# Kernel optimization log

Measured on AMD Instinct MI355X. Metric: run time of the kernel, lower is better.

## Reference

```python
import jax, jax.numpy as jnp
import numpy as np

N = 50000      # nodes
E = 800000     # edges
D_IN = 128     # irreps_in dim
SH = 16        # irreps_sh dim (lmax=3)
EA = 16        # edge_attr_dim
H = 8          # num_heads
DQ = 64        # irreps_query dim (8 per head)
DK = 64        # irreps_key dim (8 per head)
DV = 128       # irreps_out dim (16 per head)
HID = 64       # radial MLP hidden


def setup_inputs() -> dict:
    key = jax.random.key(0)
    ks = jax.random.split(key, 20)
    g = lambda k, shape, fan: jax.random.normal(k, shape, jnp.float32) / np.sqrt(fan)
    return {
        "node_attr": jax.random.normal(ks[0], (N, D_IN), jnp.float32),
        "edge_attr": jax.random.normal(ks[1], (E, EA), jnp.float32),
        "edge_sh": jax.random.normal(ks[2], (E, SH), jnp.float32),
        # h_q linear
        "Wq": g(ks[3], (D_IN, DQ), D_IN),
        # h_k conv: depthwise SH mixing, channel-mixing linear, radial MLP gate
        "Wang_k": g(ks[4], (D_IN, SH), SH),
        "Wlin_k": g(ks[5], (D_IN, DK), D_IN),
        "W1k": g(ks[6], (EA, HID), EA),
        "b1k": jnp.zeros((HID,), jnp.float32),
        "W2k": g(ks[7], (HID, DK), HID),
        # h_v conv
        "Wang_v": g(ks[8], (D_IN, SH), SH),
        "Wlin_v": g(ks[9], (D_IN, DV), D_IN),
        "W1v": g(ks[10], (EA, HID), EA),
        "b1v": jnp.zeros((HID,), jnp.float32),
        "W2v": g(ks[11], (HID, DV), HID),
        # FullyConnectedTensorProduct(query_per_head, key_per_head, '0e') -> weighted bilinear dot
        "Wdot": g(ks[12], (DQ // H, DK // H), DQ // H),
        # lin_out
        "Wout": g(ks[13], (DV, DV), DV),
        "edge_index": jax.random.randint(ks[14], (2, E), 0, N, jnp.int64),
    }


def _conv_per_edge(x_src, edge_attr, edge_sh, Wang, Wlin, W1, b1, W2):
    # depthwise tensor product of node feats with edge SH, channel mix, radial gate
    rad = jax.nn.relu(edge_attr @ W1 + b1) @ W2          # [E, Dout]
    g = edge_sh @ Wang.T                                  # [E, D_IN]
    return ((x_src * g) @ Wlin) * rad                     # [E, Dout]


def reference(node_attr, edge_attr, edge_sh, Wq, Wang_k, Wlin_k, W1k, b1k, W2k,
              Wang_v, Wlin_v, W1v, b1v, W2v, Wdot, Wout, edge_index):
    src, dst = edge_index[0], edge_index[1]
    n = node_attr.shape[0]
    e = src.shape[0]

    q = (node_attr @ Wq).reshape(n, H, DQ // H)           # [N,H,dq]
    x_src = node_attr[src]                                # gather [E,D_IN]
    k = _conv_per_edge(x_src, edge_attr, edge_sh, Wang_k, Wlin_k, W1k, b1k, W2k).reshape(e, H, DK // H)
    v = _conv_per_edge(x_src, edge_attr, edge_sh, Wang_v, Wlin_v, W1v, b1v, W2v).reshape(e, H, DV // H)

    # TP 'dot' to scalars: weighted bilinear per head
    alpha = jnp.einsum('ehq,qk,ehk->eh', q[dst], Wdot, k)  # [E,H]

    # scatter_softmax over incoming edges of each dst node
    amax = jax.ops.segment_max(alpha, dst, num_segments=n)  # [N,H]
    ealpha = jnp.exp(alpha - amax[dst])
    denom = jax.ops.segment_sum(ealpha, dst, num_segments=n)
    attn = ealpha / denom[dst]                              # [E,H]

    # weighted scatter-sum of values
    out = jax.ops.segment_sum(attn[..., None] * v, dst, num_segments=n)  # [N,H,dv]
    return out.reshape(n, DV) @ Wout
```

## Files before the change

### kernel.cpp

```cpp
#include <hip/hip_runtime.h>
#include <stdint.h>

#define NN 50000
#define NE 800000
#define STRIP 49

typedef unsigned int u32;
typedef uint16_t u16;

__device__ __forceinline__ float b2f(u16 u){ return __builtin_bit_cast(float, (u32)((u32)u << 16)); }
__device__ __forceinline__ float b2f_lo(u32 p){ return __builtin_bit_cast(float, p << 16); }
__device__ __forceinline__ float b2f_hi(u32 p){ return __builtin_bit_cast(float, p & 0xffff0000u); }
__device__ __forceinline__ u32 f2b_bits(float f){ u32 u = __builtin_bit_cast(u32, f); return (u + 0x7fffu + ((u >> 16) & 1u)) >> 16; }
__device__ __forceinline__ u16 f2b(float f){ return (u16)f2b_bits(f); }
__device__ __forceinline__ u32 packb(float lo, float hi){ return f2b_bits(lo) | (f2b_bits(hi) << 16); }

typedef __bf16 bf16x2 __attribute__((ext_vector_type(2)));
#if defined(__has_builtin)
#if __has_builtin(__builtin_amdgcn_fdot2_f32_bf16)
#define HAVE_DOT2_BUILTIN 1
#endif
#endif

#ifdef HAVE_DOT2_BUILTIN
__device__ __forceinline__ float dot2b(u32 a, u32 b, float c){
  return __builtin_amdgcn_fdot2_f32_bf16(__builtin_bit_cast(bf16x2, a),
                                         __builtin_bit_cast(bf16x2, b), c, false);
}
#else
__device__ __forceinline__ float dot2b(u32 a, u32 b, float c){
  c = fmaf(b2f_lo(a), b2f_lo(b), c);
  return fmaf(b2f_hi(a), b2f_hi(b), c);
}
#endif

typedef __attribute__((ext_vector_type(8))) short short8;
typedef __attribute__((ext_vector_type(4))) float f32x4;
__device__ __forceinline__ f32x4 mf32(uint4 a, uint4 b, f32x4 c){
  return __builtin_amdgcn_mfma_f32_16x16x32_bf16(
      __builtin_bit_cast(short8, a), __builtin_bit_cast(short8, b), c, 0, 0, 0);
}

#define OFF_WANG_V 0
#define OFF_W1_V   5120
#define OFF_WLIN_V 7680
#define OFF_W2_V   25088
#define OFF_WANG_K 34304
#define OFF_W1_K   39424
#define OFF_WLIN_K 41984
#define OFF_W2_K   50688
#define OFF_WOUT   55296
#define OFF_WQD    72704
#define WT_TOTAL   81408

__global__ __launch_bounds__(256) void zero_kernel(int* __restrict__ counts,
                                                   int* __restrict__ edge_ids)
{
  int i = blockIdx.x * 256 + threadIdx.x;
  if (i < NN) counts[i] = 0;
  if (i < NE) edge_ids[i] = 0;
}

__global__ __launch_bounds__(256) void prep_w_kernel(
    const float* __restrict__ Wang_v, const float* __restrict__ W1_v,
    const float* __restrict__ Wlin_v, const float* __restrict__ W2_v,
    const float* __restrict__ Wang_k, const float* __restrict__ W1_k,
    const float* __restrict__ Wlin_k, const float* __restrict__ W2_k,
    const float* __restrict__ Wout, const float* __restrict__ Wq,
    const float* __restrict__ Wdot,
    u16* __restrict__ wt)
{
  int idx = blockIdx.x * 256 + threadIdx.x;
  if (idx >= WT_TOTAL) return;
  float val = 0.f;
  if (idx < OFF_W1_V) {
    int l = idx - OFF_WANG_V, n = l / 40, k = l % 40;
    if (k < 16) val = Wang_v[n * 16 + k];
  } else if (idx < OFF_WLIN_V) {
    int l = idx - OFF_W1_V, n = l / 40, k = l % 40;
    if (k < 16) val = W1_v[k * 64 + n];
  } else if (idx < OFF_W2_V) {
    int l = idx - OFF_WLIN_V, n = l / 136, k = l % 136;
    if (k < 128) val = Wlin_v[k * 128 + n];
  } else if (idx < OFF_WANG_K) {
    int l = idx - OFF_W2_V, n = l / 72, k = l % 72;
    if (k < 64) val = W2_v[k * 128 + n];
  } else if (idx < OFF_W1_K) {
    int l = idx - OFF_WANG_K, n = l / 40, k = l % 40;
    if (k < 16) val = Wang_k[n * 16 + k];
  } else if (idx < OFF_WLIN_K) {
    int l = idx - OFF_W1_K, n = l / 40, k = l % 40;
    if (k < 16) val = W1_k[k * 64 + n];
  } else if (idx < OFF_W2_K) {
    int l = idx - OFF_WLIN_K, n = l / 136, k = l % 136;
    if (k < 128) val = Wlin_k[k * 64 + n];
  } else if (idx < OFF_WOUT) {
    int l = idx - OFF_W2_K, n = l / 72, k = l % 72;
    if (k < 64) val = W2_k[k * 64 + n];
  } else if (idx < OFF_WQD) {
    int l = idx - OFF_WOUT, n = l / 136, k = l % 136;
    if (k < 128) val = Wout[k * 128 + n];
  } else {
    int l = idx - OFF_WQD, n = l / 136, k = l % 136;
    if (k < 128) {
      int h = n >> 3, r = n & 7;
      float s = 0.f;
#pragma unroll
      for (int i = 0; i < 8; ++i) s += Wq[k * 64 + h * 8 + i] * Wdot[i * 8 + r];
      val = s;
    }
  }
  wt[idx] = f2b(val);
}

__global__ __launch_bounds__(256) void qw_kernel(const float* __restrict__ node_attr,
                                                 const u16* __restrict__ wt,
                                                 u16* __restrict__ qw)
{
  __shared__ __align__(16) u16 sX[64 * 136];
  uint4* sX4 = (uint4*)sX;
  u32* sX32 = (u32*)sX;
  const uint4* wt4 = (const uint4*)wt;
  const int tid = threadIdx.x, wv = tid >> 6, lane = tid & 63, lq = lane >> 4, ln = lane & 15;
  const int n0 = blockIdx.x * 64;
  uint4 rB[4];
#pragma unroll
  for (int ks = 0; ks < 4; ++ks) rB[ks] = wt4[9088 + (wv * 16 + ln) * 17 + ks * 4 + lq];
  {
    int row = tid >> 2, q4 = tid & 3;
    int n = n0 + row;
    bool valid = n < NN;
    const float4* xp = (const float4*)(node_attr + (size_t)(valid ? n : 0) * 128);
#pragma unroll
    for (int i = 0; i < 8; ++i) {
      float4 v = valid ? xp[q4 * 8 + i] : make_float4(0.f, 0.f, 0.f, 0.f);
      sX32[row * 68 + (q4 * 8 + i) * 2]     = packb(v.x, v.y);
      sX32[row * 68 + (q4 * 8 + i) * 2 + 1] = packb(v.z, v.w);
    }
  }
  __syncthreads();
  const f32x4 z4 = {0.f, 0.f, 0.f, 0.f};
  int col = wv * 16 + ln;
#pragma unroll
  for (int et = 0; et < 4; ++et) {
    f32x4 acc = z4;
#pragma unroll
    for (int ks = 0; ks < 4; ++ks) acc = mf32(sX4[(et * 16 + ln) * 17 + ks * 4 + lq], rB[ks], acc);
#pragma unroll
    for (int r = 0; r < 4; ++r) {
      int rr = n0 + et * 16 + lq * 4 + r;
      if (rr < NN) qw[(size_t)rr * 64 + col] = f2b(acc[r]);
    }
  }
}

__global__ __launch_bounds__(256, 2) void conv_fused_kernel(
    const float* __restrict__ node_attr, const float* __restrict__ edge_attr,
    const float* __restrict__ edge_sh, const int* __restrict__ edge_index,
    const float* __restrict__ b1v, const float* __restrict__ b1k,
    const u16* __restrict__ wt, const u16* __restrict__ qw,
    u16* __restrict__ v_out, float* __restrict__ alpha)
{
  __shared__ __align__(16) u16 sE[5120];
  __shared__ __align__(16) u16 sTv[64 * 136];
  __shared__ __align__(16) u16 sTk[64 * 136];
  __shared__ __align__(16) u16 sHv[64 * 72];
  __shared__ __align__(16) u16 sHk[64 * 72];
  uint4* sE4 = (uint4*)sE;   u32* sE32 = (u32*)sE;
  uint4* sTv4 = (uint4*)sTv; uint4* sTk4 = (uint4*)sTk;
  uint4* sHv4 = (uint4*)sHv; uint4* sHk4 = (uint4*)sHk;
  const uint4* wt4 = (const uint4*)wt;

  const int tid = threadIdx.x;
  const int wv = tid >> 6, lane = tid & 63, lq = lane >> 4, ln = lane & 15;
  const int e0 = blockIdx.x * 64;
  const int nA = wv * 16 + ln, nB = (wv + 4) * 16 + ln;

  int el = tid >> 2, p = tid & 3;
  int dq = edge_index[NE + e0 + el]; if ((u32)dq >= NN) dq = 0;
  const uint4* qptr = (const uint4*)(qw + (size_t)dq * 64 + p * 16);
  uint4 q0 = qptr[0], q1 = qptr[1];

  uint4 rWangV0 = wt4[nA * 5 + lq],        rWangV1 = wt4[nB * 5 + lq];
  uint4 rW1V    = wt4[640 + nA * 5 + lq];
  uint4 rWangK0 = wt4[4288 + nA * 5 + lq], rWangK1 = wt4[4288 + nB * 5 + lq];
  uint4 rW1K    = wt4[4928 + nA * 5 + lq];
  uint4 rWlinV[2][4], rWlinK[4], rW2V[2][2], rW2K[2];
#pragma unroll
  for (int ks = 0; ks < 4; ++ks) {
    rWlinV[0][ks] = wt4[960 + nA * 17 + ks * 4 + lq];
    rWlinV[1][ks] = wt4[960 + nB * 17 + ks * 4 + lq];
    rWlinK[ks]    = wt4[5248 + nA * 17 + ks * 4 + lq];
  }
#pragma unroll
  for (int ks = 0; ks < 2; ++ks) {
    rW2V[0][ks] = wt4[3136 + nA * 9 + ks * 4 + lq];
    rW2V[1][ks] = wt4[3136 + nB * 9 + ks * 4 + lq];
    rW2K[ks]    = wt4[6336 + nA * 9 + ks * 4 + lq];
  }
  float biasV = b1v[nA], biasK = b1k[nA];

  int srcs[4][4];
#pragma unroll
  for (int et = 0; et < 4; ++et)
#pragma unroll
    for (int r = 0; r < 4; ++r) {
      int s = edge_index[e0 + et * 16 + lq * 4 + r];
      if ((u32)s >= NN) s = 0;
      srcs[et][r] = s;
    }
  float xf[2][4][4];
#pragma unroll
  for (int c = 0; c < 2; ++c) {
    int col = (wv + 4 * c) * 16 + ln;
#pragma unroll
    for (int et = 0; et < 4; ++et)
#pragma unroll
      for (int r = 0; r < 4; ++r)
        xf[c][et][r] = node_attr[(size_t)srcs[et][r] * 128 + col];
  }

  {
    int r = tid >> 2, kq = tid & 3;
    float4 ea = ((const float4*)(edge_attr + (size_t)(e0 + r) * 16))[kq];
    sE32[r * 20 + kq * 2]     = packb(ea.x, ea.y);
    sE32[r * 20 + kq * 2 + 1] = packb(ea.z, ea.w);
    sE32[r * 20 + 8 + kq]  = 0;
    sE32[r * 20 + 12 + kq] = 0;
    float4 sh = ((const float4*)(edge_sh + (size_t)(e0 + r) * 16))[kq];
    sE32[1280 + r * 20 + kq * 2]     = packb(sh.x, sh.y);
    sE32[1280 + r * 20 + kq * 2 + 1] = packb(sh.z, sh.w);
    sE32[1280 + r * 20 + 8 + kq]  = 0;
    sE32[1280 + r * 20 + 12 + kq] = 0;
  }
  __syncthreads();

  const f32x4 z4 = {0.f, 0.f, 0.f, 0.f};
#pragma unroll
  for (int et = 0; et < 4; ++et) {
    uint4 aE = sE4[(et * 16 + ln) * 5 + lq];
    uint4 aS = sE4[320 + (et * 16 + ln) * 5 + lq];
    f32x4 hv = mf32(aE, rW1V, z4);
    f32x4 hk = mf32(aE, rW1K, z4);
    f32x4 t0v = mf32(aS, rWangV0, z4);
    f32x4 t1v = mf32(aS, rWangV1, z4);
    f32x4 t0k = mf32(aS, rWangK0, z4);
    f32x4 t1k = mf32(aS, rWangK1, z4);
    int rowb = et * 16 + lq * 4;
#pragma unroll
    for (int r = 0; r < 4; ++r) {
      sHv[(rowb + r) * 72 + nA] = f2b(fmaxf(hv[r] + biasV, 0.f));
      sHk[(rowb + r) * 72 + nA] = f2b(fmaxf(hk[r] + biasK, 0.f));
      sTv[(rowb + r) * 136 + nA] = f2b(t0v[r] * xf[0][et][r]);
      sTv[(rowb + r) * 136 + nB] = f2b(t1v[r] * xf[1][et][r]);
      sTk[(rowb + r) * 136 + nA] = f2b(t0k[r] * xf[0][et][r]);
      sTk[(rowb + r) * 136 + nB] = f2b(t1k[r] * xf[1][et][r]);
    }
  }
  __syncthreads();

  f32x4 a1v[2][4], a2v[2][4], a1k[4], a2k[4];
#pragma unroll
  for (int et = 0; et < 4; ++et) {
    int ar = et * 16 + ln;
    f32x4 acc;
    acc = z4;
#pragma unroll
    for (int ks = 0; ks < 4; ++ks) acc = mf32(sTv4[ar * 17 + ks * 4 + lq], rWlinV[0][ks], acc);
    a1v[0][et] = acc;
    acc = z4;
#pragma unroll
    for (int ks = 0; ks < 4; ++ks) acc = mf32(sTv4[ar * 17 + ks * 4 + lq], rWlinV[1][ks], acc);
    a1v[1][et] = acc;
    acc = z4;
#pragma unroll
    for (int ks = 0; ks < 4; ++ks) acc = mf32(sTk4[ar * 17 + ks * 4 + lq], rWlinK[ks], acc);
    a1k[et] = acc;
    acc = z4;
#pragma unroll
    for (int ks = 0; ks < 2; ++ks) acc = mf32(sHv4[ar * 9 + ks * 4 + lq], rW2V[0][ks], acc);
    a2v[0][et] = acc;
    acc = z4;
#pragma unroll
    for (int ks = 0; ks < 2; ++ks) acc = mf32(sHv4[ar * 9 + ks * 4 + lq], rW2V[1][ks], acc);
    a2v[1][et] = acc;
    acc = z4;
#pragma unroll
    for (int ks = 0; ks < 2; ++ks) acc = mf32(sHk4[ar * 9 + ks * 4 + lq], rW2K[ks], acc);
    a2k[et] = acc;
  }
  __syncthreads();

#pragma unroll
  for (int et = 0; et < 4; ++et) {
    int rowb = et * 16 + lq * 4;
#pragma unroll
    for (int r = 0; r < 4; ++r) {
      sTv[(rowb + r) * 136 + nA] = f2b(a1v[0][et][r] * a2v[0][et][r]);
      sTv[(rowb + r) * 136 + nB] = f2b(a1v[1][et][r] * a2v[1][et][r]);
      sE[(rowb + r) * 72 + nA]   = f2b(a1k[et][r] * a2k[et][r]);
    }
  }
  __syncthreads();

  {
    int row = tid >> 2, seg = tid & 3;
    uint4* gp = (uint4*)(v_out + (size_t)(e0 + row) * 128);
#pragma unroll
    for (int i = 0; i < 4; ++i) gp[seg * 4 + i] = sTv4[row * 17 + seg * 4 + i];
  }
  {
    uint4 k0 = sE4[el * 9 + p * 2];
    uint4 k1 = sE4[el * 9 + p * 2 + 1];
    float a0 = 0.f, a1 = 0.f;
    a0 = dot2b(q0.x, k0.x, a0); a0 = dot2b(q0.y, k0.y, a0);
    a0 = dot2b(q0.z, k0.z, a0); a0 = dot2b(q0.w, k0.w, a0);
    a1 = dot2b(q1.x, k1.x, a1); a1 = dot2b(q1.y, k1.y, a1);
    a1 = dot2b(q1.z, k1.z, a1); a1 = dot2b(q1.w, k1.w, a1);
    ((float2*)(alpha + (size_t)(e0 + el) * 8))[p] = make_float2(a0, a1);
  }
}

__global__ __launch_bounds__(256) void count_kernel(const int* __restrict__ edge_index,
                                                    int* __restrict__ counts)
{
  int e = blockIdx.x * 256 + threadIdx.x;
  if (e < NE) { int d = edge_index[NE + e]; if ((u32)d >= NN) d = 0; atomicAdd(&counts[d], 1); }
}

__global__ __launch_bounds__(1024) void scan_kernel(const int* __restrict__ counts,
                                                    int* __restrict__ row_ptr,
                                                    int* __restrict__ cursor)
{
  __shared__ int s[1024];
  int tid = threadIdx.x;
  int base = tid * STRIP;
  int sum = 0;
  for (int i = 0; i < STRIP; ++i) { int idx = base + i; sum += (idx < NN) ? counts[idx] : 0; }
  s[tid] = sum;
  __syncthreads();
  for (int off = 1; off < 1024; off <<= 1) {
    int v = s[tid];
    int add = (tid >= off) ? s[tid - off] : 0;
    __syncthreads();
    s[tid] = v + add;
    __syncthreads();
  }
  int running = (tid == 0) ? 0 : s[tid - 1];
  for (int i = 0; i < STRIP; ++i) {
    int idx = base + i;
    if (idx < NN) { row_ptr[idx] = running; cursor[idx] = running; running += counts[idx]; }
  }
  if (tid == 1023) row_ptr[NN] = running;
}

__global__ __launch_bounds__(256) void fill_kernel(const int* __restrict__ edge_index,
                                                   int* __restrict__ cursor,
                                                   int* __restrict__ edge_ids)
{
  int e = blockIdx.x * 256 + threadIdx.x;
  if (e < NE) {
    int dst = edge_index[NE + e]; if ((u32)dst >= NN) dst = 0;
    int pos = atomicAdd(&cursor[dst], 1);
    if ((u32)pos < NE) edge_ids[pos] = e;
  }
}

#define OUPD(aa, ww)                                                   \
  { float mn = fmaxf(m, (aa));                                         \
    float sc = __expf(m - mn);                                         \
    float pw = __expf((aa) - mn);                                      \
    l = l * sc + pw;                                                   \
    accA = accA * sc + pw * b2f_lo(ww);                                \
    accB = accB * sc + pw * b2f_hi(ww);                                \
    m = mn; }

__global__ __launch_bounds__(256) void out_kernel(
    const int* __restrict__ row_ptr, const int* __restrict__ edge_ids,
    const float* __restrict__ alpha, const u16* __restrict__ v_e,
    const u16* __restrict__ wt, float* __restrict__ out)
{
  __shared__ __align__(16) u16 sAgg[16 * 136];
  u32* sAgg32 = (u32*)sAgg;
  uint4* sAgg4 = (uint4*)sAgg;
  const uint4* wt4 = (const uint4*)wt;
  const u32* v32 = (const u32*)v_e;
  const int tid = threadIdx.x, wv = tid >> 6, lane = tid & 63, lq = lane >> 4, ln = lane & 15;
  const f32x4 z4 = {0.f, 0.f, 0.f, 0.f};
  uint4 rWT[2][4];
#pragma unroll
  for (int c = 0; c < 2; ++c) {
    int n = (wv * 2 + c) * 16 + ln;
#pragma unroll
    for (int ks = 0; ks < 4; ++ks) rWT[c][ks] = wt4[6912 + n * 17 + ks * 4 + lq];
  }
  const int hh = lane >> 3;
  const int grp = blockIdx.x;
#pragma unroll 1
  for (int i = 0; i < 4; ++i) {
    int n = grp * 16 + wv * 4 + i;
    int beg = row_ptr[n], end = row_ptr[n + 1];
    if (beg < 0) beg = 0; if (beg > NE) beg = NE;
    if (end < beg) end = beg; if (end > NE) end = NE;
    int deg = end - beg;
    float m = -3.0e38f, l = 0.f, accA = 0.f, accB = 0.f;
    int j = 0;
#pragma unroll 1
    for (; j + 4 <= deg; j += 4) {
      int e0 = edge_ids[beg + j],     e1 = edge_ids[beg + j + 1];
      int e2 = edge_ids[beg + j + 2], e3 = edge_ids[beg + j + 3];
      if ((u32)e0 >= NE) e0 = 0; if ((u32)e1 >= NE) e1 = 0;
      if ((u32)e2 >= NE) e2 = 0; if ((u32)e3 >= NE) e3 = 0;
      float a0 = alpha[(size_t)e0 * 8 + hh]; u32 w0 = v32[(size_t)e0 * 64 + lane];
      float a1 = alpha[(size_t)e1 * 8 + hh]; u32 w1 = v32[(size_t)e1 * 64 + lane];
      float a2 = alpha[(size_t)e2 * 8 + hh]; u32 w2 = v32[(size_t)e2 * 64 + lane];
      float a3 = alpha[(size_t)e3 * 8 + hh]; u32 w3 = v32[(size_t)e3 * 64 + lane];
      OUPD(a0, w0); OUPD(a1, w1); OUPD(a2, w2); OUPD(a3, w3);
    }
#pragma unroll 1
    for (; j < deg; ++j) {
      int e = edge_ids[beg + j]; if ((u32)e >= NE) e = 0;
      float a = alpha[(size_t)e * 8 + hh]; u32 w = v32[(size_t)e * 64 + lane];
      OUPD(a, w);
    }
    float inv = (l > 0.f) ? (1.f / l) : 0.f;
    accA *= inv; accB *= inv;
    sAgg32[(wv * 4 + i) * 68 + lane] = packb(accA, accB);
  }
  __syncthreads();
#pragma unroll
  for (int c = 0; c < 2; ++c) {
    f32x4 acc = z4;
#pragma unroll
    for (int ks = 0; ks < 4; ++ks) acc = mf32(sAgg4[ln * 17 + ks * 4 + lq], rWT[c][ks], acc);
    int col = (wv * 2 + c) * 16 + ln;
#pragma unroll
    for (int r = 0; r < 4; ++r)
      out[(size_t)(grp * 16 + lq * 4 + r) * 128 + col] = acc[r];
  }
}

extern "C" void kernel_launch(void* const* d_in, const int* in_sizes, int n_in,
                              void* d_out, int out_size, void* d_ws, size_t ws_size,
                              hipStream_t stream)
{
  const float* node_attr = (const float*)d_in[0];
  const float* edge_attr = (const float*)d_in[1];
  const float* edge_sh   = (const float*)d_in[2];
  const float* Wq        = (const float*)d_in[3];
  const float* Wang_k    = (const float*)d_in[4];
  const float* Wlin_k    = (const float*)d_in[5];
  const float* W1k       = (const float*)d_in[6];
  const float* b1k       = (const float*)d_in[7];
  const float* W2k       = (const float*)d_in[8];
  const float* Wang_v    = (const float*)d_in[9];
  const float* Wlin_v    = (const float*)d_in[10];
  const float* W1v       = (const float*)d_in[11];
  const float* b1v       = (const float*)d_in[12];
  const float* W2v       = (const float*)d_in[13];
  const float* Wdot      = (const float*)d_in[14];
  const float* Wout      = (const float*)d_in[15];
  const int* edge_index  = (const int*)d_in[16];
  float* out = (float*)d_out;

  char* ws = (char*)d_ws;
  u16*   v_e      = (u16*)(ws + 0);
  float* alpha    = (float*)(ws + 204800000);
  u16*   qw       = (u16*)(ws + 230400000);
  int*   counts   = (int*)(ws + 236800000);
  int*   row_ptr  = (int*)(ws + 237000064);
  int*   cursor   = (int*)(ws + 237200128);
  int*   edge_ids = (int*)(ws + 237400192);
  u16*   wt       = (u16*)(ws + 240600192);

  zero_kernel<<<dim3((NE + 255) / 256), dim3(256), 0, stream>>>(counts, edge_ids);
  prep_w_kernel<<<dim3((WT_TOTAL + 255) / 256), dim3(256), 0, stream>>>(
      Wang_v, W1v, Wlin_v, W2v, Wang_k, W1k, Wlin_k, W2k, Wout, Wq, Wdot, wt);
  qw_kernel<<<dim3((NN + 63) / 64), dim3(256), 0, stream>>>(node_attr, wt, qw);
  conv_fused_kernel<<<dim3(NE / 64), dim3(256), 0, stream>>>(
      node_attr, edge_attr, edge_sh, edge_index, b1v, b1k, wt, qw, v_e, alpha);
  count_kernel<<<dim3((NE + 255) / 256), dim3(256), 0, stream>>>(edge_index, counts);
  scan_kernel<<<dim3(1), dim3(1024), 0, stream>>>(counts, row_ptr, cursor);
  fill_kernel<<<dim3((NE + 255) / 256), dim3(256), 0, stream>>>(edge_index, cursor, edge_ids);
  out_kernel<<<dim3(3125), dim3(256), 0, stream>>>(row_ptr, edge_ids, alpha, v_e, wt, out);
}
```

Baseline: 669.8 us.

## Serialize K and V conv phases to cut LDS and registers for higher occupancy

Restructures the fused conv kernel so the key and value branches run one after the other, reusing a single set of shared-memory buffers (combined edge_attr/edge_sh tile, one T and one H buffer) and loading weights into registers only within each phase. Edge attributes and SH are packed into one 32-wide tile, and the Wang weights are relaid to occupy the upper k-slots so one MFMA operand serves both the radial and angular products. The launch bound rises from 2 to 4 blocks per CU to use the lower LDS and register footprint. In exchange it adds more barriers and serial phases per block, and the query gather moves to the end of the kernel, where its latency is no longer hidden behind the earlier work.

```diff
diff --git a/kernel.cpp b/kernel.cpp
--- a/kernel.cpp
+++ b/kernel.cpp
@@ -75,7 +75,7 @@
   float val = 0.f;
   if (idx < OFF_W1_V) {
     int l = idx - OFF_WANG_V, n = l / 40, k = l % 40;
-    if (k < 16) val = Wang_v[n * 16 + k];
+    if (k >= 16 && k < 32) val = Wang_v[n * 16 + (k - 16)];
   } else if (idx < OFF_WLIN_V) {
     int l = idx - OFF_W1_V, n = l / 40, k = l % 40;
     if (k < 16) val = W1_v[k * 64 + n];
@@ -87,7 +87,7 @@
     if (k < 64) val = W2_v[k * 128 + n];
   } else if (idx < OFF_W1_K) {
     int l = idx - OFF_WANG_K, n = l / 40, k = l % 40;
-    if (k < 16) val = Wang_k[n * 16 + k];
+    if (k >= 16 && k < 32) val = Wang_k[n * 16 + (k - 16)];
   } else if (idx < OFF_WLIN_K) {
     int l = idx - OFF_W1_K, n = l / 40, k = l % 40;
     if (k < 16) val = W1_k[k * 64 + n];
@@ -154,21 +154,19 @@
   }
 }
 
-__global__ __launch_bounds__(256, 2) void conv_fused_kernel(
+__global__ __launch_bounds__(256, 4) void conv_fused_kernel(
     const float* __restrict__ node_attr, const float* __restrict__ edge_attr,
     const float* __restrict__ edge_sh, const int* __restrict__ edge_index,
     const float* __restrict__ b1v, const float* __restrict__ b1k,
     const u16* __restrict__ wt, const u16* __restrict__ qw,
     u16* __restrict__ v_out, float* __restrict__ alpha)
 {
-  __shared__ __align__(16) u16 sE[5120];
-  __shared__ __align__(16) u16 sTv[64 * 136];
-  __shared__ __align__(16) u16 sTk[64 * 136];
-  __shared__ __align__(16) u16 sHv[64 * 72];
-  __shared__ __align__(16) u16 sHk[64 * 72];
-  uint4* sE4 = (uint4*)sE;   u32* sE32 = (u32*)sE;
-  uint4* sTv4 = (uint4*)sTv; uint4* sTk4 = (uint4*)sTk;
-  uint4* sHv4 = (uint4*)sHv; uint4* sHk4 = (uint4*)sHk;
+  __shared__ __align__(16) u16 sC[64 * 40];
+  __shared__ __align__(16) u16 sT[64 * 136];
+  __shared__ __align__(16) u16 sH[64 * 72];
+  uint4* sC4 = (uint4*)sC; u32* sC32 = (u32*)sC;
+  uint4* sT4 = (uint4*)sT;
+  uint4* sH4 = (uint4*)sH;
   const uint4* wt4 = (const uint4*)wt;
 
   const int tid = threadIdx.x;
@@ -176,30 +174,6 @@
   const int e0 = blockIdx.x * 64;
   const int nA = wv * 16 + ln, nB = (wv + 4) * 16 + ln;
 
-  int el = tid >> 2, p = tid & 3;
-  int dq = edge_index[NE + e0 + el]; if ((u32)dq >= NN) dq = 0;
-  const uint4* qptr = (const uint4*)(qw + (size_t)dq * 64 + p * 16);
-  uint4 q0 = qptr[0], q1 = qptr[1];
-
-  uint4 rWangV0 = wt4[nA * 5 + lq],        rWangV1 = wt4[nB * 5 + lq];
-  uint4 rW1V    = wt4[640 + nA * 5 + lq];
-  uint4 rWangK0 = wt4[4288 + nA * 5 + lq], rWangK1 = wt4[4288 + nB * 5 + lq];
-  uint4 rW1K    = wt4[4928 + nA * 5 + lq];
-  uint4 rWlinV[2][4], rWlinK[4], rW2V[2][2], rW2K[2];
-#pragma unroll
-  for (int ks = 0; ks < 4; ++ks) {
-    rWlinV[0][ks] = wt4[960 + nA * 17 + ks * 4 + lq];
-    rWlinV[1][ks] = wt4[960 + nB * 17 + ks * 4 + lq];
-    rWlinK[ks]    = wt4[5248 + nA * 17 + ks * 4 + lq];
-  }
-#pragma unroll
-  for (int ks = 0; ks < 2; ++ks) {
-    rW2V[0][ks] = wt4[3136 + nA * 9 + ks * 4 + lq];
-    rW2V[1][ks] = wt4[3136 + nB * 9 + ks * 4 + lq];
-    rW2K[ks]    = wt4[6336 + nA * 9 + ks * 4 + lq];
-  }
-  float biasV = b1v[nA], biasK = b1k[nA];
-
   int srcs[4][4];
 #pragma unroll
   for (int et = 0; et < 4; ++et)
@@ -223,95 +197,140 @@
   {
     int r = tid >> 2, kq = tid & 3;
     float4 ea = ((const float4*)(edge_attr + (size_t)(e0 + r) * 16))[kq];
-    sE32[r * 20 + kq * 2]     = packb(ea.x, ea.y);
-    sE32[r * 20 + kq * 2 + 1] = packb(ea.z, ea.w);
-    sE32[r * 20 + 8 + kq]  = 0;
-    sE32[r * 20 + 12 + kq] = 0;
+    sC32[r * 20 + kq * 2]     = packb(ea.x, ea.y);
+    sC32[r * 20 + kq * 2 + 1] = packb(ea.z, ea.w);
     float4 sh = ((const float4*)(edge_sh + (size_t)(e0 + r) * 16))[kq];
-    sE32[1280 + r * 20 + kq * 2]     = packb(sh.x, sh.y);
-    sE32[1280 + r * 20 + kq * 2 + 1] = packb(sh.z, sh.w);
-    sE32[1280 + r * 20 + 8 + kq]  = 0;
-    sE32[1280 + r * 20 + 12 + kq] = 0;
+    sC32[r * 20 + 8 + kq * 2]     = packb(sh.x, sh.y);
+    sC32[r * 20 + 8 + kq * 2 + 1] = packb(sh.z, sh.w);
   }
   __syncthreads();
 
   const f32x4 z4 = {0.f, 0.f, 0.f, 0.f};
-#pragma unroll
-  for (int et = 0; et < 4; ++et) {
-    uint4 aE = sE4[(et * 16 + ln) * 5 + lq];
-    uint4 aS = sE4[320 + (et * 16 + ln) * 5 + lq];
-    f32x4 hv = mf32(aE, rW1V, z4);
-    f32x4 hk = mf32(aE, rW1K, z4);
-    f32x4 t0v = mf32(aS, rWangV0, z4);
-    f32x4 t1v = mf32(aS, rWangV1, z4);
-    f32x4 t0k = mf32(aS, rWangK0, z4);
-    f32x4 t1k = mf32(aS, rWangK1, z4);
-    int rowb = et * 16 + lq * 4;
-#pragma unroll
-    for (int r = 0; r < 4; ++r) {
-      sHv[(rowb + r) * 72 + nA] = f2b(fmaxf(hv[r] + biasV, 0.f));
-      sHk[(rowb + r) * 72 + nA] = f2b(fmaxf(hk[r] + biasK, 0.f));
-      sTv[(rowb + r) * 136 + nA] = f2b(t0v[r] * xf[0][et][r]);
-      sTv[(rowb + r) * 136 + nB] = f2b(t1v[r] * xf[1][et][r]);
-      sTk[(rowb + r) * 136 + nA] = f2b(t0k[r] * xf[0][et][r]);
-      sTk[(rowb + r) * 136 + nB] = f2b(t1k[r] * xf[1][et][r]);
-    }
-  }
-  __syncthreads();
-
-  f32x4 a1v[2][4], a2v[2][4], a1k[4], a2k[4];
-#pragma unroll
-  for (int et = 0; et < 4; ++et) {
-    int ar = et * 16 + ln;
-    f32x4 acc;
-    acc = z4;
-#pragma unroll
-    for (int ks = 0; ks < 4; ++ks) acc = mf32(sTv4[ar * 17 + ks * 4 + lq], rWlinV[0][ks], acc);
-    a1v[0][et] = acc;
-    acc = z4;
-#pragma unroll
-    for (int ks = 0; ks < 4; ++ks) acc = mf32(sTv4[ar * 17 + ks * 4 + lq], rWlinV[1][ks], acc);
-    a1v[1][et] = acc;
-    acc = z4;
-#pragma unroll
-    for (int ks = 0; ks < 4; ++ks) acc = mf32(sTk4[ar * 17 + ks * 4 + lq], rWlinK[ks], acc);
-    a1k[et] = acc;
-    acc = z4;
-#pragma unroll
-    for (int ks = 0; ks < 2; ++ks) acc = mf32(sHv4[ar * 9 + ks * 4 + lq], rW2V[0][ks], acc);
-    a2v[0][et] = acc;
-    acc = z4;
-#pragma unroll
-    for (int ks = 0; ks < 2; ++ks) acc = mf32(sHv4[ar * 9 + ks * 4 + lq], rW2V[1][ks], acc);
-    a2v[1][et] = acc;
-    acc = z4;
-#pragma unroll
-    for (int ks = 0; ks < 2; ++ks) acc = mf32(sHk4[ar * 9 + ks * 4 + lq], rW2K[ks], acc);
-    a2k[et] = acc;
-  }
-  __syncthreads();
-
+  u32 kp[4][2];
+  {
+    uint4 rW1K    = wt4[4928 + nA * 5 + lq];
+    uint4 rWangK0 = wt4[4288 + nA * 5 + lq];
+    uint4 rWangK1 = wt4[4288 + nB * 5 + lq];
+    float biasK = b1k[nA];
+#pragma unroll
+    for (int et = 0; et < 4; ++et) {
+      uint4 aC = sC4[(et * 16 + ln) * 5 + lq];
+      f32x4 h  = mf32(aC, rW1K, z4);
+      f32x4 t0 = mf32(aC, rWangK0, z4);
+      f32x4 t1 = mf32(aC, rWangK1, z4);
+      int rowb = et * 16 + lq * 4;
+#pragma unroll
+      for (int r = 0; r < 4; ++r) {
+        sH[(rowb + r) * 72 + nA]  = f2b(fmaxf(h[r] + biasK, 0.f));
+        sT[(rowb + r) * 136 + nA] = f2b(t0[r] * xf[0][et][r]);
+        sT[(rowb + r) * 136 + nB] = f2b(t1[r] * xf[1][et][r]);
+      }
+    }
+  }
+  __syncthreads();
+  {
+    uint4 rWlinK[4], rW2K[2];
+#pragma unroll
+    for (int ks = 0; ks < 4; ++ks) rWlinK[ks] = wt4[5248 + nA * 17 + ks * 4 + lq];
+#pragma unroll
+    for (int ks = 0; ks < 2; ++ks) rW2K[ks] = wt4[6336 + nA * 9 + ks * 4 + lq];
+#pragma unroll
+    for (int et = 0; et < 4; ++et) {
+      int ar = et * 16 + ln;
+      f32x4 a1 = z4, a2 = z4;
+#pragma unroll
+      for (int ks = 0; ks < 4; ++ks) a1 = mf32(sT4[ar * 17 + ks * 4 + lq], rWlinK[ks], a1);
+#pragma unroll
+      for (int ks = 0; ks < 2; ++ks) a2 = mf32(sH4[ar * 9 + ks * 4 + lq], rW2K[ks], a2);
+      kp[et][0] = packb(a1[0] * a2[0], a1[1] * a2[1]);
+      kp[et][1] = packb(a1[2] * a2[2], a1[3] * a2[3]);
+    }
+  }
+  __syncthreads();
+  u32 vp[2][4][2];
+  {
+    uint4 rW1V    = wt4[640 + nA * 5 + lq];
+    uint4 rWangV0 = wt4[nA * 5 + lq];
+    uint4 rWangV1 = wt4[nB * 5 + lq];
+    float biasV = b1v[nA];
+#pragma unroll
+    for (int et = 0; et < 4; ++et) {
+      uint4 aC = sC4[(et * 16 + ln) * 5 + lq];
+      f32x4 h  = mf32(aC, rW1V, z4);
+      f32x4 t0 = mf32(aC, rWangV0, z4);
+      f32x4 t1 = mf32(aC, rWangV1, z4);
+      int rowb = et * 16 + lq * 4;
+#pragma unroll
+      for (int r = 0; r < 4; ++r) {
+        sH[(rowb + r) * 72 + nA]  = f2b(fmaxf(h[r] + biasV, 0.f));
+        sT[(rowb + r) * 136 + nA] = f2b(t0[r] * xf[0][et][r]);
+        sT[(rowb + r) * 136 + nB] = f2b(t1[r] * xf[1][et][r]);
+      }
+    }
+  }
+  __syncthreads();
+  {
+    uint4 rWlinV0[4], rWlinV1[4], rW2V0[2], rW2V1[2];
+#pragma unroll
+    for (int ks = 0; ks < 4; ++ks) {
+      rWlinV0[ks] = wt4[960 + nA * 17 + ks * 4 + lq];
+      rWlinV1[ks] = wt4[960 + nB * 17 + ks * 4 + lq];
+    }
+#pragma unroll
+    for (int ks = 0; ks < 2; ++ks) {
+      rW2V0[ks] = wt4[3136 + nA * 9 + ks * 4 + lq];
+      rW2V1[ks] = wt4[3136 + nB * 9 + ks * 4 + lq];
+    }
+#pragma unroll
+    for (int et = 0; et < 4; ++et) {
+      int ar = et * 16 + ln;
+      f32x4 a10 = z4, a11 = z4, a20 = z4, a21 = z4;
+#pragma unroll
+      for (int ks = 0; ks < 4; ++ks) {
+        uint4 t = sT4[ar * 17 + ks * 4 + lq];
+        a10 = mf32(t, rWlinV0[ks], a10);
+        a11 = mf32(t, rWlinV1[ks], a11);
+      }
+#pragma unroll
+      for (int ks = 0; ks < 2; ++ks) {
+        uint4 hf = sH4[ar * 9 + ks * 4 + lq];
+        a20 = mf32(hf, rW2V0[ks], a20);
+        a21 = mf32(hf, rW2V1[ks], a21);
+      }
+      vp[0][et][0] = packb(a10[0] * a20[0], a10[1] * a20[1]);
+      vp[0][et][1] = packb(a10[2] * a20[2], a10[3] * a20[3]);
+      vp[1][et][0] = packb(a11[0] * a21[0], a11[1] * a21[1]);
+      vp[1][et][1] = packb(a11[2] * a21[2], a11[3] * a21[3]);
+    }
+  }
+  __syncthreads();
 #pragma unroll
   for (int et = 0; et < 4; ++et) {
     int rowb = et * 16 + lq * 4;
 #pragma unroll
     for (int r = 0; r < 4; ++r) {
-      sTv[(rowb + r) * 136 + nA] = f2b(a1v[0][et][r] * a2v[0][et][r]);
-      sTv[(rowb + r) * 136 + nB] = f2b(a1v[1][et][r] * a2v[1][et][r]);
-      sE[(rowb + r) * 72 + nA]   = f2b(a1k[et][r] * a2k[et][r]);
-    }
-  }
-  __syncthreads();
-
+      u32 kv = kp[et][r >> 1];
+      u32 v0 = vp[0][et][r >> 1];
+      u32 v1 = vp[1][et][r >> 1];
+      sH[(rowb + r) * 72 + nA]  = (r & 1) ? (u16)(kv >> 16) : (u16)kv;
+      sT[(rowb + r) * 136 + nA] = (r & 1) ? (u16)(v0 >> 16) : (u16)v0;
+      sT[(rowb + r) * 136 + nB] = (r & 1) ? (u16)(v1 >> 16) : (u16)v1;
+    }
+  }
+  __syncthreads();
   {
     int row = tid >> 2, seg = tid & 3;
     uint4* gp = (uint4*)(v_out + (size_t)(e0 + row) * 128);
 #pragma unroll
-    for (int i = 0; i < 4; ++i) gp[seg * 4 + i] = sTv4[row * 17 + seg * 4 + i];
-  }
-  {
-    uint4 k0 = sE4[el * 9 + p * 2];
-    uint4 k1 = sE4[el * 9 + p * 2 + 1];
+    for (int i = 0; i < 4; ++i) gp[seg * 4 + i] = sT4[row * 17 + seg * 4 + i];
+  }
+  {
+    int el = tid >> 2, p = tid & 3;
+    int dq = edge_index[NE + e0 + el]; if ((u32)dq >= NN) dq = 0;
+    const uint4* qptr = (const uint4*)(qw + (size_t)dq * 64 + p * 16);
+    uint4 q0 = qptr[0], q1 = qptr[1];
+    uint4 k0 = sH4[el * 9 + p * 2];
+    uint4 k1 = sH4[el * 9 + p * 2 + 1];
     float a0 = 0.f, a1 = 0.f;
     a0 = dot2b(q0.x, k0.x, a0); a0 = dot2b(q0.y, k0.y, a0);
     a0 = dot2b(q0.z, k0.z, a0); a0 = dot2b(q0.w, k0.w, a0);
```

New measurement: 686.6 us. 2.5% more time.

## Stage gathered node rows in LDS and pack edge_attr/sh into one operand

Applied to the files above, without the earlier changes.

The per-lane scalar gather of node_attr into registers is replaced by a cooperative float4 row gather, converted to bf16 and staged in shared memory. That buffer is then reused in place for the value path. edge_attr and edge_sh are packed into one K=32 MFMA operand, with the weight prep zero-padding the Wang blocks into the upper K half. The sE buffer is dropped and sHk is reused for the key output, which lowers LDS use. The cost is rounding node features to bf16 earlier and extra LDS traffic.

```diff
diff --git a/kernel.cpp b/kernel.cpp
--- a/kernel.cpp
+++ b/kernel.cpp
@@ -75,7 +75,7 @@
   float val = 0.f;
   if (idx < OFF_W1_V) {
     int l = idx - OFF_WANG_V, n = l / 40, k = l % 40;
-    if (k < 16) val = Wang_v[n * 16 + k];
+    if (k >= 16 && k < 32) val = Wang_v[n * 16 + (k - 16)];
   } else if (idx < OFF_WLIN_V) {
     int l = idx - OFF_W1_V, n = l / 40, k = l % 40;
     if (k < 16) val = W1_v[k * 64 + n];
@@ -87,7 +87,7 @@
     if (k < 64) val = W2_v[k * 128 + n];
   } else if (idx < OFF_W1_K) {
     int l = idx - OFF_WANG_K, n = l / 40, k = l % 40;
-    if (k < 16) val = Wang_k[n * 16 + k];
+    if (k >= 16 && k < 32) val = Wang_k[n * 16 + (k - 16)];
   } else if (idx < OFF_WLIN_K) {
     int l = idx - OFF_W1_K, n = l / 40, k = l % 40;
     if (k < 16) val = W1_k[k * 64 + n];
@@ -161,14 +161,16 @@
     const u16* __restrict__ wt, const u16* __restrict__ qw,
     u16* __restrict__ v_out, float* __restrict__ alpha)
 {
-  __shared__ __align__(16) u16 sE[5120];
-  __shared__ __align__(16) u16 sTv[64 * 136];
+  __shared__ __align__(16) u16 sC[64 * 40];
+  __shared__ __align__(16) u16 sX[64 * 136];
   __shared__ __align__(16) u16 sTk[64 * 136];
   __shared__ __align__(16) u16 sHv[64 * 72];
   __shared__ __align__(16) u16 sHk[64 * 72];
-  uint4* sE4 = (uint4*)sE;   u32* sE32 = (u32*)sE;
-  uint4* sTv4 = (uint4*)sTv; uint4* sTk4 = (uint4*)sTk;
-  uint4* sHv4 = (uint4*)sHv; uint4* sHk4 = (uint4*)sHk;
+  uint4* sC4 = (uint4*)sC; u32* sC32 = (u32*)sC;
+  uint4* sX4 = (uint4*)sX; u32* sX32 = (u32*)sX;
+  uint4* sTk4 = (uint4*)sTk;
+  uint4* sHv4 = (uint4*)sHv;
+  uint4* sHk4 = (uint4*)sHk;
   const uint4* wt4 = (const uint4*)wt;
 
   const int tid = threadIdx.x;
@@ -176,15 +178,15 @@
   const int e0 = blockIdx.x * 64;
   const int nA = wv * 16 + ln, nB = (wv + 4) * 16 + ln;
 
-  int el = tid >> 2, p = tid & 3;
+  const int el = tid >> 2, p = tid & 3;
   int dq = edge_index[NE + e0 + el]; if ((u32)dq >= NN) dq = 0;
   const uint4* qptr = (const uint4*)(qw + (size_t)dq * 64 + p * 16);
   uint4 q0 = qptr[0], q1 = qptr[1];
 
+  uint4 rW1V    = wt4[640 + nA * 5 + lq];
+  uint4 rW1K    = wt4[4928 + nA * 5 + lq];
   uint4 rWangV0 = wt4[nA * 5 + lq],        rWangV1 = wt4[nB * 5 + lq];
-  uint4 rW1V    = wt4[640 + nA * 5 + lq];
   uint4 rWangK0 = wt4[4288 + nA * 5 + lq], rWangK1 = wt4[4288 + nB * 5 + lq];
-  uint4 rW1K    = wt4[4928 + nA * 5 + lq];
   uint4 rWlinV[2][4], rWlinK[4], rW2V[2][2], rW2K[2];
 #pragma unroll
   for (int ks = 0; ks < 4; ++ks) {
@@ -200,61 +202,54 @@
   }
   float biasV = b1v[nA], biasK = b1k[nA];
 
-  int srcs[4][4];
-#pragma unroll
-  for (int et = 0; et < 4; ++et)
-#pragma unroll
-    for (int r = 0; r < 4; ++r) {
-      int s = edge_index[e0 + et * 16 + lq * 4 + r];
-      if ((u32)s >= NN) s = 0;
-      srcs[et][r] = s;
-    }
-  float xf[2][4][4];
-#pragma unroll
-  for (int c = 0; c < 2; ++c) {
-    int col = (wv + 4 * c) * 16 + ln;
-#pragma unroll
-    for (int et = 0; et < 4; ++et)
-#pragma unroll
-      for (int r = 0; r < 4; ++r)
-        xf[c][et][r] = node_attr[(size_t)srcs[et][r] * 128 + col];
-  }
-
   {
     int r = tid >> 2, kq = tid & 3;
     float4 ea = ((const float4*)(edge_attr + (size_t)(e0 + r) * 16))[kq];
-    sE32[r * 20 + kq * 2]     = packb(ea.x, ea.y);
-    sE32[r * 20 + kq * 2 + 1] = packb(ea.z, ea.w);
-    sE32[r * 20 + 8 + kq]  = 0;
-    sE32[r * 20 + 12 + kq] = 0;
+    sC32[r * 20 + kq * 2]     = packb(ea.x, ea.y);
+    sC32[r * 20 + kq * 2 + 1] = packb(ea.z, ea.w);
     float4 sh = ((const float4*)(edge_sh + (size_t)(e0 + r) * 16))[kq];
-    sE32[1280 + r * 20 + kq * 2]     = packb(sh.x, sh.y);
-    sE32[1280 + r * 20 + kq * 2 + 1] = packb(sh.z, sh.w);
-    sE32[1280 + r * 20 + 8 + kq]  = 0;
-    sE32[1280 + r * 20 + 12 + kq] = 0;
+    sC32[r * 20 + 8 + kq * 2]     = packb(sh.x, sh.y);
+    sC32[r * 20 + 8 + kq * 2 + 1] = packb(sh.z, sh.w);
+  }
+  {
+    int g = tid >> 3, j = tid & 7;
+#pragma unroll
+    for (int rr = 0; rr < 2; ++rr) {
+      int row = g + rr * 32;
+      int s = edge_index[e0 + row]; if ((u32)s >= NN) s = 0;
+      const float4* xp = (const float4*)(node_attr + (size_t)s * 128);
+#pragma unroll
+      for (int c = 0; c < 4; ++c) {
+        float4 v = xp[c * 8 + j];
+        sX32[row * 68 + c * 16 + j * 2]     = packb(v.x, v.y);
+        sX32[row * 68 + c * 16 + j * 2 + 1] = packb(v.z, v.w);
+      }
+    }
   }
   __syncthreads();
 
   const f32x4 z4 = {0.f, 0.f, 0.f, 0.f};
 #pragma unroll
   for (int et = 0; et < 4; ++et) {
-    uint4 aE = sE4[(et * 16 + ln) * 5 + lq];
-    uint4 aS = sE4[320 + (et * 16 + ln) * 5 + lq];
-    f32x4 hv = mf32(aE, rW1V, z4);
-    f32x4 hk = mf32(aE, rW1K, z4);
-    f32x4 t0v = mf32(aS, rWangV0, z4);
-    f32x4 t1v = mf32(aS, rWangV1, z4);
-    f32x4 t0k = mf32(aS, rWangK0, z4);
-    f32x4 t1k = mf32(aS, rWangK1, z4);
+    uint4 aC = sC4[(et * 16 + ln) * 5 + lq];
+    f32x4 hv  = mf32(aC, rW1V, z4);
+    f32x4 hk  = mf32(aC, rW1K, z4);
+    f32x4 t0v = mf32(aC, rWangV0, z4);
+    f32x4 t1v = mf32(aC, rWangV1, z4);
+    f32x4 t0k = mf32(aC, rWangK0, z4);
+    f32x4 t1k = mf32(aC, rWangK1, z4);
     int rowb = et * 16 + lq * 4;
 #pragma unroll
     for (int r = 0; r < 4; ++r) {
-      sHv[(rowb + r) * 72 + nA] = f2b(fmaxf(hv[r] + biasV, 0.f));
-      sHk[(rowb + r) * 72 + nA] = f2b(fmaxf(hk[r] + biasK, 0.f));
-      sTv[(rowb + r) * 136 + nA] = f2b(t0v[r] * xf[0][et][r]);
-      sTv[(rowb + r) * 136 + nB] = f2b(t1v[r] * xf[1][et][r]);
-      sTk[(rowb + r) * 136 + nA] = f2b(t0k[r] * xf[0][et][r]);
-      sTk[(rowb + r) * 136 + nB] = f2b(t1k[r] * xf[1][et][r]);
+      int row = rowb + r;
+      float xA = b2f(sX[row * 136 + nA]);
+      float xB = b2f(sX[row * 136 + nB]);
+      sHv[row * 72 + nA]  = f2b(fmaxf(hv[r] + biasV, 0.f));
+      sHk[row * 72 + nA]  = f2b(fmaxf(hk[r] + biasK, 0.f));
+      sTk[row * 136 + nA] = f2b(t0k[r] * xA);
+      sTk[row * 136 + nB] = f2b(t1k[r] * xB);
+      sX[row * 136 + nA]  = f2b(t0v[r] * xA);
+      sX[row * 136 + nB]  = f2b(t1v[r] * xB);
     }
   }
   __syncthreads();
@@ -266,11 +261,11 @@
     f32x4 acc;
     acc = z4;
 #pragma unroll
-    for (int ks = 0; ks < 4; ++ks) acc = mf32(sTv4[ar * 17 + ks * 4 + lq], rWlinV[0][ks], acc);
+    for (int ks = 0; ks < 4; ++ks) acc = mf32(sX4[ar * 17 + ks * 4 + lq], rWlinV[0][ks], acc);
     a1v[0][et] = acc;
     acc = z4;
 #pragma unroll
-    for (int ks = 0; ks < 4; ++ks) acc = mf32(sTv4[ar * 17 + ks * 4 + lq], rWlinV[1][ks], acc);
+    for (int ks = 0; ks < 4; ++ks) acc = mf32(sX4[ar * 17 + ks * 4 + lq], rWlinV[1][ks], acc);
     a1v[1][et] = acc;
     acc = z4;
 #pragma unroll
@@ -296,9 +291,10 @@
     int rowb = et * 16 + lq * 4;
 #pragma unroll
     for (int r = 0; r < 4; ++r) {
-      sTv[(rowb + r) * 136 + nA] = f2b(a1v[0][et][r] * a2v[0][et][r]);
-      sTv[(rowb + r) * 136 + nB] = f2b(a1v[1][et][r] * a2v[1][et][r]);
-      sE[(rowb + r) * 72 + nA]   = f2b(a1k[et][r] * a2k[et][r]);
+      int row = rowb + r;
+      sX[row * 136 + nA] = f2b(a1v[0][et][r] * a2v[0][et][r]);
+      sX[row * 136 + nB] = f2b(a1v[1][et][r] * a2v[1][et][r]);
+      sHk[row * 72 + nA] = f2b(a1k[et][r] * a2k[et][r]);
     }
   }
   __syncthreads();
@@ -307,11 +303,11 @@
     int row = tid >> 2, seg = tid & 3;
     uint4* gp = (uint4*)(v_out + (size_t)(e0 + row) * 128);
 #pragma unroll
-    for (int i = 0; i < 4; ++i) gp[seg * 4 + i] = sTv4[row * 17 + seg * 4 + i];
+    for (int i = 0; i < 4; ++i) gp[seg * 4 + i] = sX4[row * 17 + seg * 4 + i];
   }
   {
-    uint4 k0 = sE4[el * 9 + p * 2];
-    uint4 k1 = sE4[el * 9 + p * 2 + 1];
+    uint4 k0 = sHk4[el * 9 + p * 2];
+    uint4 k1 = sHk4[el * 9 + p * 2 + 1];
     float a0 = 0.f, a1 = 0.f;
     a0 = dot2b(q0.x, k0.x, a0); a0 = dot2b(q0.y, k0.y, a0);
     a0 = dot2b(q0.z, k0.z, a0); a0 = dot2b(q0.w, k0.w, a0);
```

Result: slower. 685.1 us (+2.3%).
